# Kernel tuning notes

Measured on AMD Instinct MI355X. Metric: run time of the kernel, lower is better.

## Reference

```python
import jax, jax.numpy as jnp
import numpy as np

S, D, H = 2048, 2048, 16
HD = D // H  # head dim = 128
LN_EPS = 1e-5


def _ln(x, g, b):
    mu = jnp.mean(x, axis=-1, keepdims=True)
    var = jnp.var(x, axis=-1, keepdims=True)
    return (x - mu) / jnp.sqrt(var + LN_EPS) * g + b


def setup_inputs() -> dict:
    key = jax.random.key(0)
    ks = jax.random.split(key, 8)
    B = 2
    s = 0.02  # weight init scale
    return {
        "x": jax.random.normal(ks[0], (B, S, D), jnp.float32),
        "Wq": jax.random.normal(ks[1], (D, D), jnp.float32) * s,
        "bq": jnp.zeros((D,), jnp.float32),
        "Wk": jax.random.normal(ks[2], (D, D), jnp.float32) * s,
        "bk": jnp.zeros((D,), jnp.float32),
        "Wv": jax.random.normal(ks[3], (D, D), jnp.float32) * s,
        "bv": jnp.zeros((D,), jnp.float32),
        "Wo": jax.random.normal(ks[4], (D, D), jnp.float32) * s,
        "bo": jnp.zeros((D,), jnp.float32),
        "ln1_g": jnp.ones((D,), jnp.float32),
        "ln1_b": jnp.zeros((D,), jnp.float32),
        "ln2_g": jnp.ones((D,), jnp.float32),
        "ln2_b": jnp.zeros((D,), jnp.float32),
        "W1": jax.random.normal(ks[5], (4 * D, D), jnp.float32) * s,
        "b1": jnp.zeros((4 * D,), jnp.float32),
        "W2": jax.random.normal(ks[6], (D, 4 * D), jnp.float32) * s,
        "b2": jnp.zeros((D,), jnp.float32),
    }


def reference(x, Wq, bq, Wk, bk, Wv, bv, Wo, bo,
              ln1_g, ln1_b, ln2_g, ln2_b, W1, b1, W2, b2):
    causal = jnp.tril(jnp.ones((S, S), bool))  # [S, S] lower-triangular mask
    neg = jnp.finfo(x.dtype).min
    inv_sqrt_hd = 1.0 / jnp.sqrt(jnp.asarray(HD, x.dtype))

    def block(xs):  # xs: [S, D] (equinox module is per-sequence; vmapped over batch)
        h = _ln(xs, ln1_g, ln1_b)
        q = (h @ Wq.T + bq).reshape(S, H, HD)
        k = (h @ Wk.T + bk).reshape(S, H, HD)
        v = (h @ Wv.T + bv).reshape(S, H, HD)
        logits = jnp.einsum('shd,Shd->hsS', q, k) * inv_sqrt_hd
        logits = jnp.where(causal, logits, neg)
        attn = jax.nn.softmax(logits, axis=-1)
        o = jnp.einsum('hsS,Shd->shd', attn, v).reshape(S, D)
        h = h + (o @ Wo.T + bo)          # residual of post-ln1 value (as in source)
        h2 = _ln(h, ln2_g, ln2_b)
        m = jax.nn.gelu(h2 @ W1.T + b1) @ W2.T + b2
        return h2 + m                    # residual of post-ln2 value (as in source)

    return jax.vmap(block)(x)
```

## Files before the change

kernel.cpp:

```cpp
#include <hip/hip_runtime.h>
#include <hip/hip_bf16.h>
#include <math.h>

#define DD   2048
#define SS   2048
#define HH   16
#define HDIM 128
#define BB   2
#define MM   4096
#define D4   8192

using bf16x8 = __attribute__((ext_vector_type(8))) short;
using f32x4  = __attribute__((ext_vector_type(4))) float;
using f32x16 = __attribute__((ext_vector_type(16))) float;

__device__ __forceinline__ ushort f2bf(float x) {
  uint u = __builtin_bit_cast(uint, x);
  u += 0x7FFFu + ((u >> 16) & 1u);
  return (ushort)(u >> 16);
}

__device__ __forceinline__ float gelu_f(float v) {
  float u = 0.7978845608028654f * (v + 0.044715f * v * v * v);
  float e = __expf(2.0f * u);
  float th = 1.0f - 2.0f / (e + 1.0f);
  return 0.5f * v * (1.0f + th);
}

__device__ __forceinline__ void gload_lds16(const void* g, void* l) {
  __builtin_amdgcn_global_load_lds(
      (const __attribute__((address_space(1))) void*)g,
      (__attribute__((address_space(3))) void*)l, 16, 0, 0);
}

__global__ __launch_bounds__(256) void cvt_f32_bf16(
    const float* __restrict__ in, ushort* __restrict__ out, int n4) {
  int i = blockIdx.x * 256 + threadIdx.x;
  if (i >= n4) return;
  float4 v = ((const float4*)in)[i];
  ushort4 o;
  o.x = f2bf(v.x); o.y = f2bf(v.y); o.z = f2bf(v.z); o.w = f2bf(v.w);
  ((ushort4*)out)[i] = o;
}

__global__ __launch_bounds__(256) void ln_rows(
    const float* __restrict__ in, const float* __restrict__ gam,
    const float* __restrict__ bet, float* __restrict__ outf,
    ushort* __restrict__ outb) {
  int row = blockIdx.x;
  int t = threadIdx.x;
  const float4* r4 = (const float4*)(in + (size_t)row * DD);
  float4 v0 = r4[t], v1 = r4[t + 256];
  float s = v0.x + v0.y + v0.z + v0.w + v1.x + v1.y + v1.z + v1.w;
  __shared__ float redA[4], redB[4];
  #pragma unroll
  for (int off = 32; off >= 1; off >>= 1) s += __shfl_xor(s, off);
  if ((t & 63) == 0) redA[t >> 6] = s;
  __syncthreads();
  float mean = (redA[0] + redA[1] + redA[2] + redA[3]) * (1.0f / DD);
  float d0 = v0.x - mean, d1 = v0.y - mean, d2 = v0.z - mean, d3 = v0.w - mean;
  float d4 = v1.x - mean, d5 = v1.y - mean, d6 = v1.z - mean, d7 = v1.w - mean;
  float q = d0*d0 + d1*d1 + d2*d2 + d3*d3 + d4*d4 + d5*d5 + d6*d6 + d7*d7;
  #pragma unroll
  for (int off = 32; off >= 1; off >>= 1) q += __shfl_xor(q, off);
  if ((t & 63) == 0) redB[t >> 6] = q;
  __syncthreads();
  float var = (redB[0] + redB[1] + redB[2] + redB[3]) * (1.0f / DD);
  float rstd = rsqrtf(var + 1e-5f);
  const float4* g4 = (const float4*)gam;
  const float4* b4 = (const float4*)bet;
  float4 g0 = g4[t], g1 = g4[t + 256], bb0 = b4[t], bb1 = b4[t + 256];
  float4 y0, y1;
  y0.x = d0 * rstd * g0.x + bb0.x;  y0.y = d1 * rstd * g0.y + bb0.y;
  y0.z = d2 * rstd * g0.z + bb0.z;  y0.w = d3 * rstd * g0.w + bb0.w;
  y1.x = d4 * rstd * g1.x + bb1.x;  y1.y = d5 * rstd * g1.y + bb1.y;
  y1.z = d6 * rstd * g1.z + bb1.z;  y1.w = d7 * rstd * g1.w + bb1.w;
  float4* of4 = (float4*)(outf + (size_t)row * DD);
  of4[t] = y0; of4[t + 256] = y1;
  ushort4 u0, u1;
  u0.x = f2bf(y0.x); u0.y = f2bf(y0.y); u0.z = f2bf(y0.z); u0.w = f2bf(y0.w);
  u1.x = f2bf(y1.x); u1.y = f2bf(y1.y); u1.z = f2bf(y1.z); u1.w = f2bf(y1.w);
  ushort4* ob4 = (ushort4*)(outb + (size_t)row * DD);
  ob4[t] = u0; ob4[t + 256] = u1;
}

template <int OMODE, bool GELU_, bool RES_>
__global__ __launch_bounds__(512, 2) void gemm2(
    const ushort* __restrict__ A, const ushort* __restrict__ Bt,
    const float* __restrict__ pb0, const float* __restrict__ pb1,
    const float* __restrict__ pb2, const float* __restrict__ res,
    void* __restrict__ Cout, int M, int N, int K) {
  extern __shared__ __align__(16) ushort smem[];
  const int nbm = M >> 8, nbn = N >> 7;
  const int nwg = nbm * nbn;
  int wg = blockIdx.x;
  int wg2 = (wg & 7) * (nwg >> 3) + (wg >> 3);
  int bm = wg2 % nbm, bn = wg2 / nbm;
  int m0 = bm << 8, n0 = bn << 7;
  int t = threadIdx.x, lane = t & 63, w = t >> 6;
  int wm = w >> 2, wn = w & 3;
  int lr = lane & 15, lg = lane >> 4;

  auto stage = [&](int kt, int slot) {
    int k0 = kt << 6;
    ushort* lA = smem + slot * 24576;
    ushort* lB = lA + 16384;
    #pragma unroll
    for (int r = 0; r < 4; r++) {
      int idx = (r << 9) + t;
      int row = idx >> 3, ch = idx & 7;
      gload_lds16(A + (size_t)(m0 + row) * K + k0 + ((ch ^ (row & 7)) << 3),
                  lA + idx * 8);
    }
    #pragma unroll
    for (int r = 0; r < 2; r++) {
      int idx = (r << 9) + t;
      int row = idx >> 3, ch = idx & 7;
      gload_lds16(Bt + (size_t)(n0 + row) * K + k0 + ((ch ^ (row & 7)) << 3),
                  lB + idx * 8);
    }
  };

  f32x4 acc[8][2] = {};
  const int NT = K >> 6;
  stage(0, 0);
  stage(1, 1);
  int slot = 0;
  for (int kt = 0; kt < NT; ++kt) {
    __builtin_amdgcn_sched_barrier(0);
    if (kt + 1 < NT)
      asm volatile("s_waitcnt vmcnt(6) lgkmcnt(0)" ::: "memory");
    else
      asm volatile("s_waitcnt vmcnt(0) lgkmcnt(0)" ::: "memory");
    __builtin_amdgcn_s_barrier();
    __builtin_amdgcn_sched_barrier(0);
    if (kt + 2 < NT) {
      int s2 = slot + 2; if (s2 >= 3) s2 -= 3;
      stage(kt + 2, s2);
    }
    const ushort* lA = smem + slot * 24576;
    const ushort* lB = lA + 16384;
    bf16x8 af[8][2], bfr[2][2];
    #pragma unroll
    for (int mi = 0; mi < 8; mi++) {
      int row = wm * 128 + mi * 16 + lr;
      #pragma unroll
      for (int ks = 0; ks < 2; ks++)
        af[mi][ks] = *(const bf16x8*)
            &lA[row * 64 + (((ks * 4 + lg) ^ (row & 7)) << 3)];
    }
    #pragma unroll
    for (int ni = 0; ni < 2; ni++) {
      int row = wn * 32 + ni * 16 + lr;
      #pragma unroll
      for (int ks = 0; ks < 2; ks++)
        bfr[ni][ks] = *(const bf16x8*)
            &lB[row * 64 + (((ks * 4 + lg) ^ (row & 7)) << 3)];
    }
    __builtin_amdgcn_s_setprio(1);
    #pragma unroll
    for (int ks = 0; ks < 2; ks++)
      #pragma unroll
      for (int mi = 0; mi < 8; mi++)
        #pragma unroll
        for (int ni = 0; ni < 2; ni++)
          acc[mi][ni] = __builtin_amdgcn_mfma_f32_16x16x32_bf16(
              af[mi][ks], bfr[ni][ks], acc[mi][ni], 0, 0, 0);
    __builtin_amdgcn_s_setprio(0);
    slot = (slot + 1 == 3) ? 0 : slot + 1;
  }

  if (OMODE == 3) {
    int seg = n0 >> 11;
    const float* pb = (seg == 0) ? pb0 : (seg == 1) ? pb1 : pb2;
    int c0 = n0 & 2047;
    float bv[2];
    #pragma unroll
    for (int ni = 0; ni < 2; ni++) bv[ni] = pb[c0 + wn * 32 + ni * 16 + lr];
    if (seg < 2) {
      ushort* q_or_k = (ushort*)Cout + (size_t)seg * MM * DD;
      #pragma unroll
      for (int mi = 0; mi < 8; mi++) {
        #pragma unroll
        for (int r = 0; r < 4; r++) {
          int m = m0 + wm * 128 + mi * 16 + lg * 4 + r;
          #pragma unroll
          for (int ni = 0; ni < 2; ni++) {
            int col = c0 + wn * 32 + ni * 16 + lr;
            q_or_k[(size_t)m * DD + col] = f2bf(acc[mi][ni][r] + bv[ni]);
          }
        }
      }
    } else {
      ushort* vT = (ushort*)Cout + (size_t)2 * MM * DD;
      #pragma unroll
      for (int mi = 0; mi < 8; mi++) {
        int mg = m0 + wm * 128 + mi * 16 + lg * 4;
        int bb_ = mg >> 11, sb = mg & 2047;
        #pragma unroll
        for (int ni = 0; ni < 2; ni++) {
          int col = c0 + wn * 32 + ni * 16 + lr;
          int h = col >> 7, d = col & 127;
          ushort4 u4;
          u4.x = f2bf(acc[mi][ni][0] + bv[ni]);
          u4.y = f2bf(acc[mi][ni][1] + bv[ni]);
          u4.z = f2bf(acc[mi][ni][2] + bv[ni]);
          u4.w = f2bf(acc[mi][ni][3] + bv[ni]);
          size_t idx = ((size_t)(bb_ * 16 + h) * 128 + d) * 2048 + sb;
          *(ushort4*)&vT[idx] = u4;
        }
      }
    }
    return;
  }

  float bv[2];
  #pragma unroll
  for (int ni = 0; ni < 2; ni++) bv[ni] = pb0[n0 + wn * 32 + ni * 16 + lr];
  #pragma unroll
  for (int mi = 0; mi < 8; mi++) {
    #pragma unroll
    for (int r = 0; r < 4; r++) {
      int m = m0 + wm * 128 + mi * 16 + lg * 4 + r;
      #pragma unroll
      for (int ni = 0; ni < 2; ni++) {
        int n = n0 + wn * 32 + ni * 16 + lr;
        size_t idx = (size_t)m * N + n;
        float v = acc[mi][ni][r] + bv[ni];
        if (RES_) v += res[idx];
        if (GELU_) v = gelu_f(v);
        if (OMODE == 1) ((ushort*)Cout)[idx] = f2bf(v);
        else            ((float*)Cout)[idx] = v;
      }
    }
  }
}

__global__ __launch_bounds__(256) void attn_fwd(
    const ushort* __restrict__ qb, const ushort* __restrict__ kb,
    const ushort* __restrict__ vTb, ushort* __restrict__ ob) {
  __shared__ ushort Ks[64 * 128];
  __shared__ ushort Vs[128 * 64];
  __shared__ ushort Ps[4][32 * 64];

  int blk = blockIdx.x;
  int i15 = blk & 15;
  int qt = (blk & 256) ? i15 : 15 - i15;
  int bh = blk >> 4;
  int b = bh >> 4, h = bh & 15;
  int q0 = qt << 7;
  int t = threadIdx.x, lane = t & 63, w = t >> 6;
  int l31 = lane & 31, hi = lane >> 5;
  const size_t base = (size_t)b * SS * DD + (size_t)h * HDIM;
  const ushort* qp = qb + base;
  const ushort* kp = kb + base;
  const ushort* vp = vTb + (size_t)bh * HDIM * SS;
  int wq0 = q0 + w * 32;
  int qg = wq0 + l31;

  bf16x8 qf[8];
  #pragma unroll
  for (int kk = 0; kk < 8; kk++)
    qf[kk] = *(const bf16x8*)(qp + (size_t)qg * DD + kk * 16 + hi * 8);

  f32x16 o[4] = {};
  float mu = -1e30f, lrow = 0.f;
  const float csc = 0.08838834764831845f * 1.4426950408889634f;

  int nIter = 2 * qt + 2;
  for (int it = 0; it < nIter; ++it) {
    int kv0 = it * 64;
    #pragma unroll
    for (int ii = 0; ii < 4; ii++) {
      int chunk = ii * 256 + t;
      int row = chunk >> 4, cc = chunk & 15;
      gload_lds16(kp + (size_t)(kv0 + row) * DD + ((cc ^ (row & 15)) << 3),
                  &Ks[chunk * 8]);
    }
    #pragma unroll
    for (int ii = 0; ii < 4; ii++) {
      int chunk = ii * 256 + t;
      int row = chunk >> 3, cc = chunk & 7;
      gload_lds16(vp + (size_t)row * SS + kv0 + ((cc ^ (row & 7)) << 3),
                  &Vs[chunk * 8]);
    }
    __syncthreads();

    if (kv0 <= wq0 + 31) {
      f32x16 s2[2] = {};
      #pragma unroll
      for (int nt = 0; nt < 2; nt++) {
        int row = nt * 32 + l31;
        #pragma unroll
        for (int kk = 0; kk < 8; kk++) {
          bf16x8 kf = *(const bf16x8*)
              &Ks[row * 128 + (((kk * 2 + hi) ^ (row & 15)) << 3)];
          s2[nt] = __builtin_amdgcn_mfma_f32_32x32x16_bf16(kf, qf[kk], s2[nt],
                                                           0, 0, 0);
        }
      }
      float mx = -3e38f;
      #pragma unroll
      for (int nt = 0; nt < 2; nt++) {
        #pragma unroll
        for (int r = 0; r < 16; r++) {
          int kvl = nt * 32 + (r & 3) + 8 * (r >> 2) + 4 * hi;
          float u = (kv0 + kvl > qg) ? -3e38f : s2[nt][r] * csc;
          s2[nt][r] = u;
          mx = fmaxf(mx, u);
        }
      }
      mx = fmaxf(mx, __shfl_xor(mx, 32));
      float mnew = fmaxf(mu, mx);
      float fr = exp2f(mu - mnew);
      mu = mnew;
      float sum = 0.f;
      #pragma unroll
      for (int nt = 0; nt < 2; nt++)
        #pragma unroll
        for (int r = 0; r < 16; r++) {
          float p = exp2f(s2[nt][r] - mnew);
          s2[nt][r] = p;
          sum += p;
        }
      sum += __shfl_xor(sum, 32);
      lrow = lrow * fr + sum;
      #pragma unroll
      for (int dt = 0; dt < 4; dt++)
        #pragma unroll
        for (int r = 0; r < 16; r++) o[dt][r] *= fr;
      #pragma unroll
      for (int nt = 0; nt < 2; nt++) {
        #pragma unroll
        for (int g2 = 0; g2 < 4; g2++) {
          ushort4 u4;
          u4.x = f2bf(s2[nt][g2 * 4 + 0]);
          u4.y = f2bf(s2[nt][g2 * 4 + 1]);
          u4.z = f2bf(s2[nt][g2 * 4 + 2]);
          u4.w = f2bf(s2[nt][g2 * 4 + 3]);
          int cp = (nt * 4 + g2) ^ (l31 & 7);
          *(ushort4*)&Ps[w][l31 * 64 + cp * 8 + hi * 4] = u4;
        }
      }
      asm volatile("s_waitcnt lgkmcnt(0)" ::: "memory");
      #pragma unroll
      for (int kk = 0; kk < 4; kk++) {
        bf16x8 pf = *(const bf16x8*)
            &Ps[w][l31 * 64 + (((kk * 2 + hi) ^ (l31 & 7)) << 3)];
        #pragma unroll
        for (int dt = 0; dt < 4; dt++) {
          int drow = dt * 32 + l31;
          bf16x8 vf = *(const bf16x8*)
              &Vs[drow * 64 + (((kk * 2 + hi) ^ (drow & 7)) << 3)];
          o[dt] = __builtin_amdgcn_mfma_f32_32x32x16_bf16(vf, pf, o[dt],
                                                          0, 0, 0);
        }
      }
    }
    __syncthreads();
  }

  float inv = 1.0f / lrow;
  #pragma unroll
  for (int dt = 0; dt < 4; dt++) {
    #pragma unroll
    for (int g2 = 0; g2 < 4; g2++) {
      ushort4 u4;
      u4.x = f2bf(o[dt][g2 * 4 + 0] * inv);
      u4.y = f2bf(o[dt][g2 * 4 + 1] * inv);
      u4.z = f2bf(o[dt][g2 * 4 + 2] * inv);
      u4.w = f2bf(o[dt][g2 * 4 + 3] * inv);
      int d = dt * 32 + 8 * g2 + 4 * hi;
      *(ushort4*)&ob[base + (size_t)qg * DD + d] = u4;
    }
  }
}

extern "C" void kernel_launch(void* const* d_in, const int* in_sizes, int n_in,
                              void* d_out, int out_size, void* d_ws,
                              size_t ws_size, hipStream_t stream) {
  const float* x    = (const float*)d_in[0];
  const float* Wq   = (const float*)d_in[1];
  const float* bq   = (const float*)d_in[2];
  const float* Wk   = (const float*)d_in[3];
  const float* bk   = (const float*)d_in[4];
  const float* Wv   = (const float*)d_in[5];
  const float* bv   = (const float*)d_in[6];
  const float* Wo   = (const float*)d_in[7];
  const float* bo   = (const float*)d_in[8];
  const float* ln1g = (const float*)d_in[9];
  const float* ln1b = (const float*)d_in[10];
  const float* ln2g = (const float*)d_in[11];
  const float* ln2b = (const float*)d_in[12];
  const float* W1   = (const float*)d_in[13];
  const float* b1   = (const float*)d_in[14];
  const float* W2   = (const float*)d_in[15];
  const float* b2   = (const float*)d_in[16];

  char* ws = (char*)d_ws;
  ushort* Wqkvb = (ushort*)(ws);
  ushort* Wob   = Wqkvb + (size_t)3 * DD * DD;
  ushort* W1b = (ushort*)(ws);
  ushort* W2b = W1b + (size_t)D4 * DD;
  ushort* qkvb = (ushort*)(ws + 67108864);
  ushort* qbf = qkvb;
  ushort* kbf = qbf + (size_t)MM * DD;
  ushort* vTt = kbf + (size_t)MM * DD;
  ushort* aob = vTt + (size_t)MM * DD;
  ushort* gb  = (ushort*)(ws + 67108864);
  float* hf  = (float*)(ws + 134217728);
  float* h2f = hf;
  ushort* hb  = (ushort*)(ws + 167772160);
  ushort* h2b = hb;
  float* h2in = (float*)(ws + 184549376);
  float* out  = (float*)d_out;

  const int LDSB = 147456;
  hipFuncSetAttribute((const void*)gemm2<3, false, false>,
                      hipFuncAttributeMaxDynamicSharedMemorySize, LDSB);
  hipFuncSetAttribute((const void*)gemm2<0, false, true>,
                      hipFuncAttributeMaxDynamicSharedMemorySize, LDSB);
  hipFuncSetAttribute((const void*)gemm2<1, true, false>,
                      hipFuncAttributeMaxDynamicSharedMemorySize, LDSB);

  dim3 blk(256);
  dim3 gblk(512);
  cvt_f32_bf16<<<DD * DD / 1024, blk, 0, stream>>>(Wq, Wqkvb, DD * DD / 4);
  cvt_f32_bf16<<<DD * DD / 1024, blk, 0, stream>>>(Wk, Wqkvb + (size_t)DD * DD, DD * DD / 4);
  cvt_f32_bf16<<<DD * DD / 1024, blk, 0, stream>>>(Wv, Wqkvb + (size_t)2 * DD * DD, DD * DD / 4);
  cvt_f32_bf16<<<DD * DD / 1024, blk, 0, stream>>>(Wo, Wob, DD * DD / 4);
  ln_rows<<<MM, blk, 0, stream>>>(x, ln1g, ln1b, hf, hb);
  gemm2<3, false, false><<<768, gblk, LDSB, stream>>>(
      hb, Wqkvb, bq, bk, bv, nullptr, qkvb, MM, 3 * DD, DD);
  attn_fwd<<<512, blk, 0, stream>>>(qbf, kbf, vTt, aob);
  gemm2<0, false, true><<<256, gblk, LDSB, stream>>>(
      aob, Wob, bo, bo, bo, hf, h2in, MM, DD, DD);
  ln_rows<<<MM, blk, 0, stream>>>(h2in, ln2g, ln2b, h2f, h2b);
  cvt_f32_bf16<<<D4 * DD / 1024, blk, 0, stream>>>(W1, W1b, D4 * DD / 4);
  cvt_f32_bf16<<<D4 * DD / 1024, blk, 0, stream>>>(W2, W2b, D4 * DD / 4);
  gemm2<1, true, false><<<1024, gblk, LDSB, stream>>>(
      h2b, W1b, b1, b1, b1, nullptr, gb, MM, D4, DD);
  gemm2<0, false, true><<<256, gblk, LDSB, stream>>>(
      gb, W2b, b2, b2, b2, h2f, out, MM, DD, D4);
}
```

Baseline: 668.1 us.

## Double-buffer attention KV, lazy softmax rescale, and use bf16 residuals

The attention kernel now double-buffers its K/V tiles in dynamic LDS, so the next tile's global-to-LDS loads overlap compute on the current one. The softmax skips the causal mask on fully visible tiles and only rescales the accumulator when the running max grows past a threshold. LayerNorm no longer writes an fp32 copy, and the GEMM residual adds now read the bf16 activations, which cuts memory traffic at the cost of residual precision. Packed bf16 stores replace per-element ushort writes.

Measured after the change: 628.7 us. 5.9% less time.

```diff
diff --git a/kernel.cpp b/kernel.cpp
--- a/kernel.cpp
+++ b/kernel.cpp
@@ -18,6 +18,12 @@
   uint u = __builtin_bit_cast(uint, x);
   u += 0x7FFFu + ((u >> 16) & 1u);
   return (ushort)(u >> 16);
+}
+__device__ __forceinline__ float bf2f(ushort u) {
+  return __builtin_bit_cast(float, (uint)u << 16);
+}
+__device__ __forceinline__ uint pkbf2(float a, float b) {
+  return (uint)f2bf(a) | ((uint)f2bf(b) << 16);
 }
 
 __device__ __forceinline__ float gelu_f(float v) {
@@ -45,8 +51,7 @@
 
 __global__ __launch_bounds__(256) void ln_rows(
     const float* __restrict__ in, const float* __restrict__ gam,
-    const float* __restrict__ bet, float* __restrict__ outf,
-    ushort* __restrict__ outb) {
+    const float* __restrict__ bet, ushort* __restrict__ outb) {
   int row = blockIdx.x;
   int t = threadIdx.x;
   const float4* r4 = (const float4*)(in + (size_t)row * DD);
@@ -75,8 +80,6 @@
   y0.z = d2 * rstd * g0.z + bb0.z;  y0.w = d3 * rstd * g0.w + bb0.w;
   y1.x = d4 * rstd * g1.x + bb1.x;  y1.y = d5 * rstd * g1.y + bb1.y;
   y1.z = d6 * rstd * g1.z + bb1.z;  y1.w = d7 * rstd * g1.w + bb1.w;
-  float4* of4 = (float4*)(outf + (size_t)row * DD);
-  of4[t] = y0; of4[t + 256] = y1;
   ushort4 u0, u1;
   u0.x = f2bf(y0.x); u0.y = f2bf(y0.y); u0.z = f2bf(y0.z); u0.w = f2bf(y0.w);
   u1.x = f2bf(y1.x); u1.y = f2bf(y1.y); u1.z = f2bf(y1.z); u1.w = f2bf(y1.w);
@@ -88,7 +91,7 @@
 __global__ __launch_bounds__(512, 2) void gemm2(
     const ushort* __restrict__ A, const ushort* __restrict__ Bt,
     const float* __restrict__ pb0, const float* __restrict__ pb1,
-    const float* __restrict__ pb2, const float* __restrict__ res,
+    const float* __restrict__ pb2, const ushort* __restrict__ res,
     void* __restrict__ Cout, int M, int N, int K) {
   extern __shared__ __align__(16) ushort smem[];
   const int nbm = M >> 8, nbn = N >> 7;
@@ -227,7 +230,7 @@
         int n = n0 + wn * 32 + ni * 16 + lr;
         size_t idx = (size_t)m * N + n;
         float v = acc[mi][ni][r] + bv[ni];
-        if (RES_) v += res[idx];
+        if (RES_) v += bf2f(res[idx]);
         if (GELU_) v = gelu_f(v);
         if (OMODE == 1) ((ushort*)Cout)[idx] = f2bf(v);
         else            ((float*)Cout)[idx] = v;
@@ -239,9 +242,10 @@
 __global__ __launch_bounds__(256) void attn_fwd(
     const ushort* __restrict__ qb, const ushort* __restrict__ kb,
     const ushort* __restrict__ vTb, ushort* __restrict__ ob) {
-  __shared__ ushort Ks[64 * 128];
-  __shared__ ushort Vs[128 * 64];
-  __shared__ ushort Ps[4][32 * 64];
+  extern __shared__ __align__(16) ushort asm_[];
+  ushort* KsB = asm_;
+  ushort* VsB = asm_ + 16384;
+  ushort* Pw  = asm_ + 32768 + (threadIdx.x >> 6) * 2048;
 
   int blk = blockIdx.x;
   int i15 = blk & 15;
@@ -263,30 +267,42 @@
   for (int kk = 0; kk < 8; kk++)
     qf[kk] = *(const bf16x8*)(qp + (size_t)qg * DD + kk * 16 + hi * 8);
 
-  f32x16 o[4] = {};
-  float mu = -1e30f, lrow = 0.f;
-  const float csc = 0.08838834764831845f * 1.4426950408889634f;
-
-  int nIter = 2 * qt + 2;
-  for (int it = 0; it < nIter; ++it) {
+  auto stageKV = [&](int it, int buf) {
     int kv0 = it * 64;
+    ushort* Kd = KsB + buf * 8192;
+    ushort* Vd = VsB + buf * 8192;
     #pragma unroll
     for (int ii = 0; ii < 4; ii++) {
       int chunk = ii * 256 + t;
       int row = chunk >> 4, cc = chunk & 15;
       gload_lds16(kp + (size_t)(kv0 + row) * DD + ((cc ^ (row & 15)) << 3),
-                  &Ks[chunk * 8]);
+                  Kd + chunk * 8);
     }
     #pragma unroll
     for (int ii = 0; ii < 4; ii++) {
       int chunk = ii * 256 + t;
       int row = chunk >> 3, cc = chunk & 7;
       gload_lds16(vp + (size_t)row * SS + kv0 + ((cc ^ (row & 7)) << 3),
-                  &Vs[chunk * 8]);
-    }
-    __syncthreads();
+                  Vd + chunk * 8);
+    }
+  };
+
+  f32x16 o[4] = {};
+  float mu = -1e30f, lrow = 0.f;
+  const float csc = 0.08838834764831845f * 1.4426950408889634f;
+
+  int nIter = 2 * qt + 2;
+  stageKV(0, 0);
+  asm volatile("s_waitcnt vmcnt(0)" ::: "memory");
+  __builtin_amdgcn_s_barrier();
+  int cur = 0;
+  for (int it = 0; it < nIter; ++it) {
+    int kv0 = it * 64;
+    if (it + 1 < nIter) stageKV(it + 1, cur ^ 1);
 
     if (kv0 <= wq0 + 31) {
+      const ushort* Kc = KsB + cur * 8192;
+      const ushort* Vc = VsB + cur * 8192;
       f32x16 s2[2] = {};
       #pragma unroll
       for (int nt = 0; nt < 2; nt++) {
@@ -294,70 +310,92 @@
         #pragma unroll
         for (int kk = 0; kk < 8; kk++) {
           bf16x8 kf = *(const bf16x8*)
-              &Ks[row * 128 + (((kk * 2 + hi) ^ (row & 15)) << 3)];
+              &Kc[row * 128 + (((kk * 2 + hi) ^ (row & 15)) << 3)];
           s2[nt] = __builtin_amdgcn_mfma_f32_32x32x16_bf16(kf, qf[kk], s2[nt],
                                                            0, 0, 0);
         }
       }
-      float mx = -3e38f;
+      bool full = (kv0 + 63 <= wq0);
+      float pm[4] = {-3e38f, -3e38f, -3e38f, -3e38f};
+      if (full) {
+        #pragma unroll
+        for (int nt = 0; nt < 2; nt++)
+          #pragma unroll
+          for (int g2 = 0; g2 < 4; g2++)
+            #pragma unroll
+            for (int i = 0; i < 4; i++) {
+              float u = s2[nt][g2 * 4 + i] * csc;
+              s2[nt][g2 * 4 + i] = u;
+              pm[i] = fmaxf(pm[i], u);
+            }
+      } else {
+        #pragma unroll
+        for (int nt = 0; nt < 2; nt++)
+          #pragma unroll
+          for (int g2 = 0; g2 < 4; g2++)
+            #pragma unroll
+            for (int i = 0; i < 4; i++) {
+              int kvl = nt * 32 + g2 * 8 + 4 * hi + i;
+              float u = (kv0 + kvl > qg) ? -3e38f : s2[nt][g2 * 4 + i] * csc;
+              s2[nt][g2 * 4 + i] = u;
+              pm[i] = fmaxf(pm[i], u);
+            }
+      }
+      float mx = fmaxf(fmaxf(pm[0], pm[1]), fmaxf(pm[2], pm[3]));
+      mx = fmaxf(mx, __shfl_xor(mx, 32));
+      if (!__all(mx - mu <= 8.0f)) {
+        float mnew = fmaxf(mu, mx);
+        float fr = exp2f(mu - mnew);
+        mu = mnew;
+        lrow *= fr;
+        #pragma unroll
+        for (int dt = 0; dt < 4; dt++)
+          #pragma unroll
+          for (int r = 0; r < 16; r++) o[dt][r] *= fr;
+      }
+      float ps[4] = {0.f, 0.f, 0.f, 0.f};
+      #pragma unroll
+      for (int nt = 0; nt < 2; nt++)
+        #pragma unroll
+        for (int g2 = 0; g2 < 4; g2++)
+          #pragma unroll
+          for (int i = 0; i < 4; i++) {
+            float p = exp2f(s2[nt][g2 * 4 + i] - mu);
+            s2[nt][g2 * 4 + i] = p;
+            ps[i] += p;
+          }
+      float sum = (ps[0] + ps[1]) + (ps[2] + ps[3]);
+      sum += __shfl_xor(sum, 32);
+      lrow += sum;
       #pragma unroll
       for (int nt = 0; nt < 2; nt++) {
         #pragma unroll
-        for (int r = 0; r < 16; r++) {
-          int kvl = nt * 32 + (r & 3) + 8 * (r >> 2) + 4 * hi;
-          float u = (kv0 + kvl > qg) ? -3e38f : s2[nt][r] * csc;
-          s2[nt][r] = u;
-          mx = fmaxf(mx, u);
-        }
-      }
-      mx = fmaxf(mx, __shfl_xor(mx, 32));
-      float mnew = fmaxf(mu, mx);
-      float fr = exp2f(mu - mnew);
-      mu = mnew;
-      float sum = 0.f;
-      #pragma unroll
-      for (int nt = 0; nt < 2; nt++)
-        #pragma unroll
-        for (int r = 0; r < 16; r++) {
-          float p = exp2f(s2[nt][r] - mnew);
-          s2[nt][r] = p;
-          sum += p;
-        }
-      sum += __shfl_xor(sum, 32);
-      lrow = lrow * fr + sum;
-      #pragma unroll
-      for (int dt = 0; dt < 4; dt++)
-        #pragma unroll
-        for (int r = 0; r < 16; r++) o[dt][r] *= fr;
-      #pragma unroll
-      for (int nt = 0; nt < 2; nt++) {
-        #pragma unroll
         for (int g2 = 0; g2 < 4; g2++) {
-          ushort4 u4;
-          u4.x = f2bf(s2[nt][g2 * 4 + 0]);
-          u4.y = f2bf(s2[nt][g2 * 4 + 1]);
-          u4.z = f2bf(s2[nt][g2 * 4 + 2]);
-          u4.w = f2bf(s2[nt][g2 * 4 + 3]);
+          uint2 u;
+          u.x = pkbf2(s2[nt][g2 * 4 + 0], s2[nt][g2 * 4 + 1]);
+          u.y = pkbf2(s2[nt][g2 * 4 + 2], s2[nt][g2 * 4 + 3]);
           int cp = (nt * 4 + g2) ^ (l31 & 7);
-          *(ushort4*)&Ps[w][l31 * 64 + cp * 8 + hi * 4] = u4;
+          *(uint2*)&Pw[l31 * 64 + cp * 8 + hi * 4] = u;
         }
       }
       asm volatile("s_waitcnt lgkmcnt(0)" ::: "memory");
       #pragma unroll
       for (int kk = 0; kk < 4; kk++) {
         bf16x8 pf = *(const bf16x8*)
-            &Ps[w][l31 * 64 + (((kk * 2 + hi) ^ (l31 & 7)) << 3)];
+            &Pw[l31 * 64 + (((kk * 2 + hi) ^ (l31 & 7)) << 3)];
         #pragma unroll
         for (int dt = 0; dt < 4; dt++) {
           int drow = dt * 32 + l31;
           bf16x8 vf = *(const bf16x8*)
-              &Vs[drow * 64 + (((kk * 2 + hi) ^ (drow & 7)) << 3)];
+              &Vc[drow * 64 + (((kk * 2 + hi) ^ (drow & 7)) << 3)];
           o[dt] = __builtin_amdgcn_mfma_f32_32x32x16_bf16(vf, pf, o[dt],
                                                           0, 0, 0);
         }
       }
     }
-    __syncthreads();
+    asm volatile("s_waitcnt vmcnt(0)" ::: "memory");
+    __builtin_amdgcn_s_barrier();
+    cur ^= 1;
   }
 
   float inv = 1.0f / lrow;
@@ -365,13 +403,11 @@
   for (int dt = 0; dt < 4; dt++) {
     #pragma unroll
     for (int g2 = 0; g2 < 4; g2++) {
-      ushort4 u4;
-      u4.x = f2bf(o[dt][g2 * 4 + 0] * inv);
-      u4.y = f2bf(o[dt][g2 * 4 + 1] * inv);
-      u4.z = f2bf(o[dt][g2 * 4 + 2] * inv);
-      u4.w = f2bf(o[dt][g2 * 4 + 3] * inv);
+      uint2 u;
+      u.x = pkbf2(o[dt][g2 * 4 + 0] * inv, o[dt][g2 * 4 + 1] * inv);
+      u.y = pkbf2(o[dt][g2 * 4 + 2] * inv, o[dt][g2 * 4 + 3] * inv);
       int d = dt * 32 + 8 * g2 + 4 * hi;
-      *(ushort4*)&ob[base + (size_t)qg * DD + d] = u4;
+      *(uint2*)&ob[base + (size_t)qg * DD + d] = u;
     }
   }
 }
@@ -408,20 +444,21 @@
   ushort* vTt = kbf + (size_t)MM * DD;
   ushort* aob = vTt + (size_t)MM * DD;
   ushort* gb  = (ushort*)(ws + 67108864);
-  float* hf  = (float*)(ws + 134217728);
-  float* h2f = hf;
   ushort* hb  = (ushort*)(ws + 167772160);
   ushort* h2b = hb;
   float* h2in = (float*)(ws + 184549376);
   float* out  = (float*)d_out;
 
   const int LDSB = 147456;
-  hipFuncSetAttribute((const void*)gemm2<3, false, false>,
+  const int LDSA = 81920;
+  (void)hipFuncSetAttribute((const void*)gemm2<3, false, false>,
                       hipFuncAttributeMaxDynamicSharedMemorySize, LDSB);
-  hipFuncSetAttribute((const void*)gemm2<0, false, true>,
+  (void)hipFuncSetAttribute((const void*)gemm2<0, false, true>,
                       hipFuncAttributeMaxDynamicSharedMemorySize, LDSB);
-  hipFuncSetAttribute((const void*)gemm2<1, true, false>,
+  (void)hipFuncSetAttribute((const void*)gemm2<1, true, false>,
                       hipFuncAttributeMaxDynamicSharedMemorySize, LDSB);
+  (void)hipFuncSetAttribute((const void*)attn_fwd,
+                      hipFuncAttributeMaxDynamicSharedMemorySize, LDSA);
 
   dim3 blk(256);
   dim3 gblk(512);
@@ -429,17 +466,17 @@
   cvt_f32_bf16<<<DD * DD / 1024, blk, 0, stream>>>(Wk, Wqkvb + (size_t)DD * DD, DD * DD / 4);
   cvt_f32_bf16<<<DD * DD / 1024, blk, 0, stream>>>(Wv, Wqkvb + (size_t)2 * DD * DD, DD * DD / 4);
   cvt_f32_bf16<<<DD * DD / 1024, blk, 0, stream>>>(Wo, Wob, DD * DD / 4);
-  ln_rows<<<MM, blk, 0, stream>>>(x, ln1g, ln1b, hf, hb);
+  ln_rows<<<MM, blk, 0, stream>>>(x, ln1g, ln1b, hb);
   gemm2<3, false, false><<<768, gblk, LDSB, stream>>>(
       hb, Wqkvb, bq, bk, bv, nullptr, qkvb, MM, 3 * DD, DD);
-  attn_fwd<<<512, blk, 0, stream>>>(qbf, kbf, vTt, aob);
+  attn_fwd<<<512, blk, LDSA, stream>>>(qbf, kbf, vTt, aob);
   gemm2<0, false, true><<<256, gblk, LDSB, stream>>>(
-      aob, Wob, bo, bo, bo, hf, h2in, MM, DD, DD);
-  ln_rows<<<MM, blk, 0, stream>>>(h2in, ln2g, ln2b, h2f, h2b);
+      aob, Wob, bo, bo, bo, hb, h2in, MM, DD, DD);
+  ln_rows<<<MM, blk, 0, stream>>>(h2in, ln2g, ln2b, h2b);
   cvt_f32_bf16<<<D4 * DD / 1024, blk, 0, stream>>>(W1, W1b, D4 * DD / 4);
   cvt_f32_bf16<<<D4 * DD / 1024, blk, 0, stream>>>(W2, W2b, D4 * DD / 4);
   gemm2<1, true, false><<<1024, gblk, LDSB, stream>>>(
       h2b, W1b, b1, b1, b1, nullptr, gb, MM, D4, DD);
   gemm2<0, false, true><<<256, gblk, LDSB, stream>>>(
-      gb, W2b, b2, b2, b2, h2f, out, MM, DD, D4);
-}
+      gb, W2b, b2, b2, b2, h2b, out, MM, DD, D4);
+}
```
